# Optimization experiments

Hardware: AMD Instinct MI355X
Metric: run time of the kernel (lower is better)

## Reference

```python
import jax, jax.numpy as jnp
import numpy as np

N = 50000      # nodes
E = 800000     # edges
DIN = 128      # input_dim
H = 128        # hidden_dim
DOUT = 64      # output_dim
G = 256        # graphs in batch
HOPS = 2       # num_hops
EPS = 1e-5     # BatchNorm eps


def setup_inputs() -> dict:
    key = jax.random.key(0)
    ks = jax.random.split(key, 16)
    w = lambda k, shape: jax.random.normal(k, shape, jnp.float32) * 0.05
    return dict(
        x=jax.random.normal(ks[0], (N, DIN), jnp.float32),
        edge_index=jax.random.randint(ks[1], (2, E), 0, N),
        batch=jnp.sort(jax.random.randint(ks[2], (N,), 0, G)),
        # preprocess FFNN (weights stored [in, out]; math == torch x @ W.T + b)
        pre_w1=w(ks[3], (DIN, H)), pre_b1=jnp.zeros((H,), jnp.float32),
        pre_w2=w(ks[4], (H, H)),   pre_b2=jnp.zeros((H,), jnp.float32),
        # per-hop GCNConv weight/bias
        conv_w=w(ks[5], (HOPS, H, H)), conv_b=jnp.zeros((HOPS, H), jnp.float32),
        # per-hop FFNN
        ffnn_w1=w(ks[6], (HOPS, H, H)), ffnn_b1=jnp.zeros((HOPS, H), jnp.float32),
        ffnn_w2=w(ks[7], (HOPS, H, H)), ffnn_b2=jnp.zeros((HOPS, H), jnp.float32),
        # per-hop BatchNorm affine params
        bn_gamma=jnp.ones((HOPS, H), jnp.float32), bn_beta=jnp.zeros((HOPS, H), jnp.float32),
        # postprocess FFNN
        post_w1=w(ks[8], (H, H)),    post_b1=jnp.zeros((H,), jnp.float32),
        post_w2=w(ks[9], (H, DOUT)), post_b2=jnp.zeros((DOUT,), jnp.float32),
    )


def _ffnn(x, w1, b1, w2, b2):
    # Linear -> GELU(exact, erf-based like nn.GELU) -> Linear
    return jax.nn.gelu(x @ w1 + b1, approximate=False) @ w2 + b2


def reference(x, edge_index, batch,
              pre_w1, pre_b1, pre_w2, pre_b2,
              conv_w, conv_b, ffnn_w1, ffnn_b1, ffnn_w2, ffnn_b2,
              bn_gamma, bn_beta,
              post_w1, post_b1, post_w2, post_b2):
    n = x.shape[0]
    loops = jnp.arange(n)
    # GCNConv default: add self-loops, symmetric D^-1/2 A D^-1/2 normalization
    src = jnp.concatenate([edge_index[0], loops])
    dst = jnp.concatenate([edge_index[1], loops])
    deg = jax.ops.segment_sum(jnp.ones(src.shape[0], x.dtype), dst, num_segments=n)
    dis = jnp.where(deg > 0, jax.lax.rsqrt(deg), 0.0)
    norm = dis[src] * dis[dst]  # [E+N]

    x = _ffnn(x, pre_w1, pre_b1, pre_w2, pre_b2)  # preprocess
    for i in range(HOPS):
        # GCNConv: (x W) gathered at src, scaled, scatter-added at dst, + bias
        xw = x @ conv_w[i]
        agg = jax.ops.segment_sum(xw[src] * norm[:, None], dst, num_segments=n) + conv_b[i]
        x = agg + x  # residual
        # BatchNorm1d (training-mode batch statistics, biased variance)
        mean = x.mean(axis=0)
        var = x.var(axis=0)
        x = (x - mean) * jax.lax.rsqrt(var + EPS) * bn_gamma[i] + bn_beta[i]
        # dropout treated as identity (deterministic reference)
        x = _ffnn(x, ffnn_w1[i], ffnn_b1[i], ffnn_w2[i], ffnn_b2[i]) + x
    # global_mean_pool over graph ids
    sums = jax.ops.segment_sum(x, batch, num_segments=G)
    cnt = jax.ops.segment_sum(jnp.ones(n, x.dtype), batch, num_segments=G)
    pooled = sums / jnp.maximum(cnt, 1.0)[:, None]
    return _ffnn(pooled, post_w1, post_b1, post_w2, post_b2)
```

## Files before the change

### kernel.cpp

```cpp
#include <hip/hip_runtime.h>
#include <hip/hip_bf16.h>
#include <math.h>

#define NN 50000
#define EE 800000
#define GG 256

typedef short bf16x8 __attribute__((ext_vector_type(8)));
typedef float f32x4 __attribute__((ext_vector_type(4)));
typedef unsigned int u32x4 __attribute__((ext_vector_type(4)));

__device__ __forceinline__ unsigned short f2bf(float x) {
    __hip_bfloat16 h = __float2bfloat16(x);
    union { __hip_bfloat16 h; unsigned short u; } c; c.h = h; return c.u;
}
__device__ __forceinline__ float bf2f(unsigned short u) {
    union { unsigned int v; float f; } t; t.v = ((unsigned int)u) << 16; return t.f;
}
__device__ __forceinline__ float gelu_f(float v) {
    return 0.5f * v * (1.0f + erff(v * 0.70710678118654752f));
}
__device__ __forceinline__ int swz(int row, int bytecol) {
    return row * 256 + (bytecol ^ ((row & 7) << 4));
}

__global__ void k_deg(const int* __restrict__ dst, int* __restrict__ degi, int E) {
    int i = blockIdx.x * blockDim.x + threadIdx.x;
    if (i < E) atomicAdd(&degi[dst[i]], 1);
}
__global__ void k_scan1(const int* __restrict__ degi, int* __restrict__ incl,
                        int* __restrict__ bsum, int N) {
    __shared__ int sm[1024];
    int t = threadIdx.x, i = blockIdx.x * 1024 + t;
    int v = (i < N) ? degi[i] : 0;
    sm[t] = v;
    __syncthreads();
    for (int off = 1; off < 1024; off <<= 1) {
        int add = (t >= off) ? sm[t - off] : 0;
        __syncthreads();
        sm[t] += add;
        __syncthreads();
    }
    if (i < N) incl[i] = sm[t];
    if (t == 1023) bsum[blockIdx.x] = sm[t];
}
__global__ void k_scan3(const int* __restrict__ incl, const int* __restrict__ degi,
                        const int* __restrict__ bsum, float* __restrict__ dis,
                        int* __restrict__ rowstart, int N, int E, int nsb) {
    __shared__ int sboff;
    int t = threadIdx.x;
    if (t < 64) {
        int nb = blockIdx.x >> 2;
        int v = (t < nb && t < nsb) ? bsum[t] : 0;
        #pragma unroll
        for (int o = 1; o < 64; o <<= 1) v += __shfl_xor(v, o, 64);
        if (t == 0) sboff = v;
    }
    __syncthreads();
    int i = blockIdx.x * 256 + t;
    if (i < N) {
        rowstart[i] = incl[i] - degi[i] + sboff;
        dis[i] = rsqrtf((float)(degi[i] + 1));
    }
    if (i == 0) rowstart[N] = E;
}
__global__ void k_fill(const int* __restrict__ src, const int* __restrict__ dst,
                       const int* __restrict__ rowstart,
                       int* __restrict__ fillc, int* __restrict__ col, int E) {
    int i = blockIdx.x * blockDim.x + threadIdx.x;
    if (i < E) {
        int s = src[i], d = dst[i];
        int pos = rowstart[d] + atomicAdd(&fillc[d], 1);
        col[pos] = s;
    }
}
__global__ void k_prepw8(const float* __restrict__ w0, const float* __restrict__ w1,
                         const float* __restrict__ w2, const float* __restrict__ w3,
                         const float* __restrict__ w4, const float* __restrict__ w5,
                         const float* __restrict__ w6, const float* __restrict__ w7,
                         unsigned short* __restrict__ Wt) {
    int b = blockIdx.x >> 6;
    const float* W = b == 0 ? w0 : b == 1 ? w1 : b == 2 ? w2 : b == 3 ? w3
                   : b == 4 ? w4 : b == 5 ? w5 : b == 6 ? w6 : w7;
    int tid = (blockIdx.x & 63) * 256 + threadIdx.x;
    int n = tid >> 7, k = tid & 127;
    *(unsigned short*)((char*)(Wt + (size_t)b * 16384) + swz(n, k * 2)) = f2bf(W[k * 128 + n]);
}

__global__ __launch_bounds__(256) void k_mm(
    const float* __restrict__ A32, const unsigned short* __restrict__ A16,
    const unsigned short* __restrict__ W1, const float* __restrict__ b1,
    const unsigned short* __restrict__ W2, const float* __restrict__ b2,
    const unsigned short* __restrict__ W3, const float* __restrict__ disv,
    const float* __restrict__ st_sum, const float* __restrict__ st_sq,
    const float* __restrict__ st_g, const float* __restrict__ st_b,
    float invN, int bn, int hasres,
    float* __restrict__ outx32, unsigned short* __restrict__ out3,
    const int* __restrict__ batch, float* __restrict__ pooled, int M)
{
    __shared__ unsigned short As[64 * 128];
    __shared__ unsigned short Ws[128 * 128];
    __shared__ float lsc[128], lsh[128];
    __shared__ float sdis[64];
    __shared__ int gid[64];
    const int tid = threadIdx.x;
    const int bm = blockIdx.x * 64;
    if (st_sum && tid < 128) {
        float m = st_sum[tid] * invN;
        float var = st_sq[tid] * invN - m * m;
        float s = st_g[tid] * rsqrtf(var + 1e-5f);
        lsc[tid] = s;
        lsh[tid] = st_b[tid] - m * s;
    }
    __syncthreads();
    {
        const uint4* srcp = (const uint4*)W1;
        uint4* dstp = (uint4*)Ws;
        for (int i = tid; i < 2048; i += 256) dstp[i] = srcp[i];
    }
    #pragma unroll
    for (int pass = 0; pass < 4; ++pass) {
        int row = pass * 16 + (tid >> 4);
        int c8 = tid & 15;
        int gr = bm + row; if (gr > M - 1) gr = M - 1;
        float vv[8];
        if (A32) {
            const float* pp = A32 + (size_t)gr * 128 + c8 * 8;
            float4 v0 = *(const float4*)pp;
            float4 v1 = *(const float4*)(pp + 4);
            vv[0] = v0.x; vv[1] = v0.y; vv[2] = v0.z; vv[3] = v0.w;
            vv[4] = v1.x; vv[5] = v1.y; vv[6] = v1.z; vv[7] = v1.w;
        } else {
            u32x4 raw = __builtin_nontemporal_load((const u32x4*)(A16 + (size_t)gr * 128 + c8 * 8));
            #pragma unroll
            for (int d = 0; d < 4; ++d) {
                vv[2 * d]     = bf2f((unsigned short)(raw[d] & 0xffff));
                vv[2 * d + 1] = bf2f((unsigned short)(raw[d] >> 16));
            }
        }
        if (bn) {
            int ch = c8 * 8;
            #pragma unroll
            for (int j = 0; j < 8; ++j) vv[j] = vv[j] * lsc[ch + j] + lsh[ch + j];
        }
        unsigned short tmp[8];
        #pragma unroll
        for (int j = 0; j < 8; ++j) tmp[j] = f2bf(vv[j]);
        *(uint4*)((char*)As + swz(row, c8 * 16)) = *(uint4*)tmp;
    }
    __syncthreads();

    const int lane = tid & 63, wid = tid >> 6;
    const int r0 = wid * 16;
    const int lrow = lane & 15;
    const int lkb = (lane >> 4) * 16;
    const int cb = lane & 15;
    const int rb = r0 + (lane >> 4) * 4;

    f32x4 acc[8];
    #pragma unroll
    for (int n = 0; n < 8; ++n) acc[n] = (f32x4){0.f, 0.f, 0.f, 0.f};
    #pragma unroll
    for (int kk = 0; kk < 4; ++kk) {
        int bc = kk * 64 + lkb;
        bf16x8 a = *(const bf16x8*)((const char*)As + swz(r0 + lrow, bc));
        #pragma unroll
        for (int n = 0; n < 8; ++n) {
            bf16x8 b = *(const bf16x8*)((const char*)Ws + swz(n * 16 + lrow, bc));
            acc[n] = __builtin_amdgcn_mfma_f32_16x16x32_bf16(a, b, acc[n], 0, 0, 0);
        }
    }
    unsigned short rres[32];
    if (hasres) {
        #pragma unroll
        for (int n = 0; n < 8; ++n)
            #pragma unroll
            for (int j = 0; j < 4; ++j)
                rres[n * 4 + j] = *(const unsigned short*)((const char*)As + swz(rb + j, (n * 16 + cb) * 2));
    }
    #pragma unroll
    for (int n = 0; n < 8; ++n) {
        int colg = n * 16 + cb;
        float bv = b1[colg];
        #pragma unroll
        for (int j = 0; j < 4; ++j) {
            float v = gelu_f(acc[n][j] + bv);
            *(unsigned short*)((char*)As + swz(rb + j, colg * 2)) = f2bf(v);
        }
    }
    __syncthreads();
    {
        const uint4* srcp = (const uint4*)W2;
        uint4* dstp = (uint4*)Ws;
        for (int i = tid; i < 2048; i += 256) dstp[i] = srcp[i];
    }
    __syncthreads();
    #pragma unroll
    for (int n = 0; n < 8; ++n) acc[n] = (f32x4){0.f, 0.f, 0.f, 0.f};
    #pragma unroll
    for (int kk = 0; kk < 4; ++kk) {
        int bc = kk * 64 + lkb;
        bf16x8 a = *(const bf16x8*)((const char*)As + swz(r0 + lrow, bc));
        #pragma unroll
        for (int n = 0; n < 8; ++n) {
            bf16x8 b = *(const bf16x8*)((const char*)Ws + swz(n * 16 + lrow, bc));
            acc[n] = __builtin_amdgcn_mfma_f32_16x16x32_bf16(a, b, acc[n], 0, 0, 0);
        }
    }
    const int dopool = (pooled != nullptr);
    float* wsf = (float*)Ws;
    #pragma unroll
    for (int n = 0; n < 8; ++n) {
        int colg = n * 16 + cb;
        float bv = b2[colg];
        #pragma unroll
        for (int j = 0; j < 4; ++j) {
            int rowg = bm + rb + j;
            float v = acc[n][j] + bv;
            if (hasres) v += bf2f(rres[n * 4 + j]);
            if (outx32 && rowg < M) outx32[(size_t)rowg * 128 + colg] = v;
            if (W3) *(unsigned short*)((char*)As + swz(rb + j, colg * 2)) = f2bf(v);
            if (dopool) wsf[(rb + j) * 128 + colg] = v;
        }
    }
    if (dopool) {
        if (tid < 64) { int r = bm + tid; gid[tid] = (r < M) ? batch[r] : -1; }
        __syncthreads();
        if (tid < 128) {
            float pacc = 0.f;
            int gcur = gid[0];
            #pragma unroll 4
            for (int r = 0; r < 64; ++r) {
                int gg = gid[r];
                if (gg != gcur) {
                    if (gcur >= 0) atomicAdd(&pooled[(size_t)gcur * 128 + tid], pacc);
                    pacc = 0.f; gcur = gg;
                }
                if (gg >= 0) pacc += wsf[r * 128 + tid];
            }
            if (gcur >= 0) atomicAdd(&pooled[(size_t)gcur * 128 + tid], pacc);
        }
        return;
    }
    if (!W3) return;
    __syncthreads();
    {
        const uint4* srcp = (const uint4*)W3;
        uint4* dstp = (uint4*)Ws;
        for (int i = tid; i < 2048; i += 256) dstp[i] = srcp[i];
        if (tid < 64) { int r = bm + tid; sdis[tid] = disv[(r < M) ? r : (M - 1)]; }
    }
    __syncthreads();
    #pragma unroll
    for (int n = 0; n < 8; ++n) acc[n] = (f32x4){0.f, 0.f, 0.f, 0.f};
    #pragma unroll
    for (int kk = 0; kk < 4; ++kk) {
        int bc = kk * 64 + lkb;
        bf16x8 a = *(const bf16x8*)((const char*)As + swz(r0 + lrow, bc));
        #pragma unroll
        for (int n = 0; n < 8; ++n) {
            bf16x8 b = *(const bf16x8*)((const char*)Ws + swz(n * 16 + lrow, bc));
            acc[n] = __builtin_amdgcn_mfma_f32_16x16x32_bf16(a, b, acc[n], 0, 0, 0);
        }
    }
    #pragma unroll
    for (int n = 0; n < 8; ++n) {
        int colg = n * 16 + cb;
        #pragma unroll
        for (int j = 0; j < 4; ++j) {
            int rowg = bm + rb + j;
            if (rowg < M) out3[(size_t)rowg * 128 + colg] = f2bf(acc[n][j] * sdis[rb + j]);
        }
    }
}

__global__ __launch_bounds__(256) void k_agg(
    const unsigned short* __restrict__ xws, const int* __restrict__ rowstart,
    const int* __restrict__ col,
    const float* __restrict__ dis, const float* __restrict__ convb,
    const float* __restrict__ x0, unsigned short* __restrict__ zbf,
    float* __restrict__ bnsum, float* __restrict__ bnsq, int N)
{
    __shared__ float redS[4][128];
    __shared__ float redQ[4][128];
    const int tid = threadIdx.x;
    const int lane = tid & 63;
    const int wid = tid >> 6;
    const int g = lane >> 4;
    const int cl = lane & 15;
    const int ch = cl * 8;
    const int wave = blockIdx.x * 4 + wid;
    const int nwaves = gridDim.x * 4;

    float cb[8];
    #pragma unroll
    for (int j = 0; j < 8; ++j) cb[j] = convb[ch + j];
    float s[8], q[8];
    #pragma unroll
    for (int j = 0; j < 8; ++j) { s[j] = 0.f; q[j] = 0.f; }

    for (int v = wave; v < N; v += nwaves) {
        const int e0 = rowstart[v], e1 = rowstart[v + 1];
        float a[8];
        #pragma unroll
        for (int j = 0; j < 8; ++j) a[j] = 0.f;
        int e = e0 + g;
        for (; e + 12 < e1; e += 16) {
            const int u0 = col[e];
            const int u1 = col[e + 4];
            const int u2 = col[e + 8];
            const int u3 = col[e + 12];
            u32x4 p0 = *(const u32x4*)(xws + (size_t)u0 * 128 + ch);
            u32x4 p1 = *(const u32x4*)(xws + (size_t)u1 * 128 + ch);
            u32x4 p2 = *(const u32x4*)(xws + (size_t)u2 * 128 + ch);
            u32x4 p3 = *(const u32x4*)(xws + (size_t)u3 * 128 + ch);
            #pragma unroll
            for (int d = 0; d < 4; ++d) {
                a[2 * d]     += bf2f((unsigned short)(p0[d] & 0xffff)) + bf2f((unsigned short)(p1[d] & 0xffff))
                              + bf2f((unsigned short)(p2[d] & 0xffff)) + bf2f((unsigned short)(p3[d] & 0xffff));
                a[2 * d + 1] += bf2f((unsigned short)(p0[d] >> 16)) + bf2f((unsigned short)(p1[d] >> 16))
                              + bf2f((unsigned short)(p2[d] >> 16)) + bf2f((unsigned short)(p3[d] >> 16));
            }
        }
        for (; e + 4 < e1; e += 8) {
            const int u0 = col[e];
            const int u1 = col[e + 4];
            u32x4 p0 = *(const u32x4*)(xws + (size_t)u0 * 128 + ch);
            u32x4 p1 = *(const u32x4*)(xws + (size_t)u1 * 128 + ch);
            #pragma unroll
            for (int d = 0; d < 4; ++d) {
                a[2 * d]     += bf2f((unsigned short)(p0[d] & 0xffff)) + bf2f((unsigned short)(p1[d] & 0xffff));
                a[2 * d + 1] += bf2f((unsigned short)(p0[d] >> 16)) + bf2f((unsigned short)(p1[d] >> 16));
            }
        }
        if (e < e1) {
            const int u = col[e];
            u32x4 p = *(const u32x4*)(xws + (size_t)u * 128 + ch);
            #pragma unroll
            for (int d = 0; d < 4; ++d) {
                a[2 * d]     += bf2f((unsigned short)(p[d] & 0xffff));
                a[2 * d + 1] += bf2f((unsigned short)(p[d] >> 16));
            }
        }
        #pragma unroll
        for (int j = 0; j < 8; ++j) {
            a[j] += __shfl_xor(a[j], 16, 64);
            a[j] += __shfl_xor(a[j], 32, 64);
        }
        if (g == 0) {
            const float dv = dis[v];
            u32x4 p = *(const u32x4*)(xws + (size_t)v * 128 + ch);
            f32x4 xa = __builtin_nontemporal_load((const f32x4*)(x0 + (size_t)v * 128 + ch));
            f32x4 xb = __builtin_nontemporal_load((const f32x4*)(x0 + (size_t)v * 128 + ch + 4));
            const float xr[8] = { xa[0], xa[1], xa[2], xa[3], xb[0], xb[1], xb[2], xb[3] };
            float zz[8];
            #pragma unroll
            for (int d = 0; d < 4; ++d) {
                zz[2 * d]     = dv * (a[2 * d]     + bf2f((unsigned short)(p[d] & 0xffff)));
                zz[2 * d + 1] = dv * (a[2 * d + 1] + bf2f((unsigned short)(p[d] >> 16)));
            }
            unsigned short zo[8];
            #pragma unroll
            for (int j = 0; j < 8; ++j) {
                zz[j] += cb[j] + xr[j];
                s[j] += zz[j];
                q[j] += zz[j] * zz[j];
                zo[j] = f2bf(zz[j]);
            }
            __builtin_nontemporal_store(*(const u32x4*)zo, (u32x4*)(zbf + (size_t)v * 128 + ch));
        }
    }
    if (g == 0) {
        #pragma unroll
        for (int j = 0; j < 8; ++j) { redS[wid][ch + j] = s[j]; redQ[wid][ch + j] = q[j]; }
    }
    __syncthreads();
    if (tid < 128) {
        float ts = redS[0][tid] + redS[1][tid] + redS[2][tid] + redS[3][tid];
        float tq = redQ[0][tid] + redQ[1][tid] + redQ[2][tid] + redQ[3][tid];
        atomicAdd(&bnsum[tid], ts);
        atomicAdd(&bnsq[tid], tq);
    }
}
__global__ __launch_bounds__(128) void k_post(
    const float* __restrict__ pooled, const int* __restrict__ batch,
    const float* __restrict__ w1, const float* __restrict__ b1,
    const float* __restrict__ w2, const float* __restrict__ b2,
    float* __restrict__ out, int N, int G)
{
    __shared__ float pr[128], hr[128];
    __shared__ int bounds[2];
    int g = blockIdx.x, t = threadIdx.x;
    if (t < 2) {
        int tgt = g + t, lo = 0, hi = N;
        while (lo < hi) { int mid = (lo + hi) >> 1; if (batch[mid] < tgt) lo = mid + 1; else hi = mid; }
        bounds[t] = lo;
    }
    __syncthreads();
    float c = fmaxf((float)(bounds[1] - bounds[0]), 1.0f);
    pr[t] = pooled[(size_t)g * 128 + t] / c;
    __syncthreads();
    float a = b1[t];
    for (int k = 0; k < 128; ++k) a += pr[k] * w1[k * 128 + t];
    hr[t] = gelu_f(a);
    __syncthreads();
    if (t < 64) {
        float o = b2[t];
        for (int k = 0; k < 128; ++k) o += hr[k] * w2[k * 64 + t];
        out[g * 64 + t] = o;
    }
}

extern "C" void kernel_launch(void* const* d_in, const int* in_sizes, int n_in,
                              void* d_out, int out_size, void* d_ws, size_t ws_size,
                              hipStream_t stream) {
    (void)in_sizes; (void)n_in; (void)out_size; (void)ws_size;
    const float* x_in    = (const float*)d_in[0];
    const int*   ei      = (const int*)d_in[1];
    const int*   batch   = (const int*)d_in[2];
    const float* pre_w1  = (const float*)d_in[3];
    const float* pre_b1  = (const float*)d_in[4];
    const float* pre_w2  = (const float*)d_in[5];
    const float* pre_b2  = (const float*)d_in[6];
    const float* conv_w  = (const float*)d_in[7];
    const float* conv_b  = (const float*)d_in[8];
    const float* ffnn_w1 = (const float*)d_in[9];
    const float* ffnn_b1 = (const float*)d_in[10];
    const float* ffnn_w2 = (const float*)d_in[11];
    const float* ffnn_b2 = (const float*)d_in[12];
    const float* bn_gamma= (const float*)d_in[13];
    const float* bn_beta = (const float*)d_in[14];
    const float* post_w1 = (const float*)d_in[15];
    const float* post_b1 = (const float*)d_in[16];
    const float* post_w2 = (const float*)d_in[17];
    const float* post_b2 = (const float*)d_in[18];
    const int* srcE = ei;
    const int* dstE = ei + EE;

    char* base = (char*)d_ws;
    size_t off = 0;
    auto carve = [&](size_t bytes) {
        char* q = base + off;
        off = (off + bytes + 255) & ~(size_t)255;
        return q;
    };
    float* xf32 = (float*)carve((size_t)NN * 128 * 4);
    unsigned short* zbf = (unsigned short*)carve((size_t)NN * 128 * 2);
    unsigned short* hbf = (unsigned short*)carve((size_t)NN * 128 * 2);
    float* dis   = (float*)carve((size_t)NN * 4);
    int*   degi  = (int*)carve((size_t)NN * 4);
    int*   fillc = (int*)carve((size_t)NN * 4);
    float* pooled= (float*)carve((size_t)GG * 128 * 4);
    float* bnstat= (float*)carve(512 * 4);
    size_t zlen  = (size_t)((char*)(bnstat + 512) - (char*)degi);
    int* incl    = (int*)carve((size_t)NN * 4);
    int* bsum    = (int*)carve(64 * 4);
    int* rowstart= (int*)carve((size_t)(NN + 1) * 4);
    int* colx    = (int*)carve((size_t)EE * 4);
    unsigned short* Wt = (unsigned short*)carve((size_t)8 * 16384 * 2);

    hipMemsetAsync(degi, 0, zlen, stream);

    const int nsb = (NN + 1023) / 1024;
    k_deg<<<(EE + 255) / 256, 256, 0, stream>>>(dstE, degi, EE);
    k_scan1<<<nsb, 1024, 0, stream>>>(degi, incl, bsum, NN);
    k_scan3<<<(NN + 255) / 256, 256, 0, stream>>>(incl, degi, bsum, dis, rowstart, NN, EE, nsb);
    k_fill<<<(EE + 255) / 256, 256, 0, stream>>>(srcE, dstE, rowstart, fillc, colx, EE);
    k_prepw8<<<512, 256, 0, stream>>>(pre_w1, pre_w2, conv_w, conv_w + 16384,
                                      ffnn_w1, ffnn_w1 + 16384, ffnn_w2, ffnn_w2 + 16384, Wt);

    const int gB = (NN + 63) / 64;
    const float invN = 1.0f / NN;
    k_mm<<<gB, 256, 0, stream>>>(x_in, nullptr, Wt + 0 * 16384, pre_b1, Wt + 1 * 16384, pre_b2,
                                 Wt + 2 * 16384, dis, nullptr, nullptr, nullptr, nullptr,
                                 invN, 0, 0, xf32, hbf, nullptr, nullptr, NN);
    k_agg<<<2048, 256, 0, stream>>>(hbf, rowstart, colx, dis, conv_b,
                                    xf32, zbf, bnstat, bnstat + 128, NN);
    k_mm<<<gB, 256, 0, stream>>>(nullptr, zbf, Wt + 4 * 16384, ffnn_b1, Wt + 6 * 16384, ffnn_b2,
                                 Wt + 3 * 16384, dis, bnstat, bnstat + 128, bn_gamma, bn_beta,
                                 invN, 1, 1, xf32, hbf, nullptr, nullptr, NN);
    k_agg<<<2048, 256, 0, stream>>>(hbf, rowstart, colx, dis, conv_b + 128,
                                    xf32, zbf, bnstat + 256, bnstat + 384, NN);
    k_mm<<<gB, 256, 0, stream>>>(nullptr, zbf, Wt + 5 * 16384, ffnn_b1 + 128, Wt + 7 * 16384, ffnn_b2 + 128,
                                 nullptr, nullptr, bnstat + 256, bnstat + 384, bn_gamma + 128, bn_beta + 128,
                                 invN, 1, 1, nullptr, nullptr, batch, pooled, NN);
    k_post<<<GG, 128, 0, stream>>>(pooled, batch, post_w1, post_b1, post_w2, post_b2,
                                   (float*)d_out, NN, GG);
}
```

Before: 381.9 us.

## Store residual stream in bf16, merge fill and weight-prep kernels, hoist agg loads

The fp32 residual activation buffer becomes bf16, which halves the bytes k_mm writes and k_agg reads for the residual. The CSR fill and weight-prep kernels are merged into one launch to save launch overhead. In k_agg the self-term and residual loads are issued before the neighbour loop so their latency overlaps the gather. The pooling path now stages results in shared memory after a barrier rather than inside the epilogue, and the bf16 residual adds rounding error.

```diff
diff --git a/kernel.cpp b/kernel.cpp
--- a/kernel.cpp
+++ b/kernel.cpp
@@ -5,6 +5,7 @@
 #define NN 50000
 #define EE 800000
 #define GG 256
+#define FILLB ((EE + 255) / 256)
 
 typedef short bf16x8 __attribute__((ext_vector_type(8)));
 typedef float f32x4 __attribute__((ext_vector_type(4)));
@@ -64,27 +65,30 @@
     }
     if (i == 0) rowstart[N] = E;
 }
-__global__ void k_fill(const int* __restrict__ src, const int* __restrict__ dst,
-                       const int* __restrict__ rowstart,
-                       int* __restrict__ fillc, int* __restrict__ col, int E) {
-    int i = blockIdx.x * blockDim.x + threadIdx.x;
-    if (i < E) {
-        int s = src[i], d = dst[i];
-        int pos = rowstart[d] + atomicAdd(&fillc[d], 1);
-        col[pos] = s;
-    }
-}
-__global__ void k_prepw8(const float* __restrict__ w0, const float* __restrict__ w1,
-                         const float* __restrict__ w2, const float* __restrict__ w3,
-                         const float* __restrict__ w4, const float* __restrict__ w5,
-                         const float* __restrict__ w6, const float* __restrict__ w7,
-                         unsigned short* __restrict__ Wt) {
-    int b = blockIdx.x >> 6;
-    const float* W = b == 0 ? w0 : b == 1 ? w1 : b == 2 ? w2 : b == 3 ? w3
-                   : b == 4 ? w4 : b == 5 ? w5 : b == 6 ? w6 : w7;
-    int tid = (blockIdx.x & 63) * 256 + threadIdx.x;
-    int n = tid >> 7, k = tid & 127;
-    *(unsigned short*)((char*)(Wt + (size_t)b * 16384) + swz(n, k * 2)) = f2bf(W[k * 128 + n]);
+__global__ void k_fillprep(const int* __restrict__ src, const int* __restrict__ dst,
+                           const int* __restrict__ rowstart, int* __restrict__ fillc,
+                           int* __restrict__ col,
+                           const float* __restrict__ w0, const float* __restrict__ w1,
+                           const float* __restrict__ w2, const float* __restrict__ w3,
+                           const float* __restrict__ w4, const float* __restrict__ w5,
+                           const float* __restrict__ w6, const float* __restrict__ w7,
+                           unsigned short* __restrict__ Wt, int E) {
+    int blk = blockIdx.x;
+    if (blk < FILLB) {
+        int i = blk * 256 + threadIdx.x;
+        if (i < E) {
+            int s = src[i], d = dst[i];
+            int pos = rowstart[d] + atomicAdd(&fillc[d], 1);
+            col[pos] = s;
+        }
+    } else {
+        int b = (blk - FILLB) >> 6;
+        const float* W = b == 0 ? w0 : b == 1 ? w1 : b == 2 ? w2 : b == 3 ? w3
+                       : b == 4 ? w4 : b == 5 ? w5 : b == 6 ? w6 : w7;
+        int tid = ((blk - FILLB) & 63) * 256 + threadIdx.x;
+        int n = tid >> 7, k = tid & 127;
+        *(unsigned short*)((char*)(Wt + (size_t)b * 16384) + swz(n, k * 2)) = f2bf(W[k * 128 + n]);
+    }
 }
 
 __global__ __launch_bounds__(256) void k_mm(
@@ -95,7 +99,7 @@
     const float* __restrict__ st_sum, const float* __restrict__ st_sq,
     const float* __restrict__ st_g, const float* __restrict__ st_b,
     float invN, int bn, int hasres,
-    float* __restrict__ outx32, unsigned short* __restrict__ out3,
+    unsigned short* __restrict__ outxbf, unsigned short* __restrict__ out3,
     const int* __restrict__ batch, float* __restrict__ pooled, int M)
 {
     __shared__ unsigned short As[64 * 128];
@@ -208,7 +212,6 @@
         }
     }
     const int dopool = (pooled != nullptr);
-    float* wsf = (float*)Ws;
     #pragma unroll
     for (int n = 0; n < 8; ++n) {
         int colg = n * 16 + cb;
@@ -218,12 +221,19 @@
             int rowg = bm + rb + j;
             float v = acc[n][j] + bv;
             if (hasres) v += bf2f(rres[n * 4 + j]);
-            if (outx32 && rowg < M) outx32[(size_t)rowg * 128 + colg] = v;
+            acc[n][j] = v;
+            if (outxbf && rowg < M) outxbf[(size_t)rowg * 128 + colg] = f2bf(v);
             if (W3) *(unsigned short*)((char*)As + swz(rb + j, colg * 2)) = f2bf(v);
-            if (dopool) wsf[(rb + j) * 128 + colg] = v;
         }
     }
     if (dopool) {
+        __syncthreads();
+        float* wsf = (float*)Ws;
+        #pragma unroll
+        for (int n = 0; n < 8; ++n)
+            #pragma unroll
+            for (int j = 0; j < 4; ++j)
+                wsf[(rb + j) * 128 + n * 16 + cb] = acc[n][j];
         if (tid < 64) { int r = bm + tid; gid[tid] = (r < M) ? batch[r] : -1; }
         __syncthreads();
         if (tid < 128) {
@@ -278,7 +288,7 @@
     const unsigned short* __restrict__ xws, const int* __restrict__ rowstart,
     const int* __restrict__ col,
     const float* __restrict__ dis, const float* __restrict__ convb,
-    const float* __restrict__ x0, unsigned short* __restrict__ zbf,
+    const unsigned short* __restrict__ x0, unsigned short* __restrict__ zbf,
     float* __restrict__ bnsum, float* __restrict__ bnsq, int N)
 {
     __shared__ float redS[4][128];
@@ -301,6 +311,14 @@
 
     for (int v = wave; v < N; v += nwaves) {
         const int e0 = rowstart[v], e1 = rowstart[v + 1];
+        float dv = 0.f;
+        u32x4 pself = (u32x4){0, 0, 0, 0};
+        u32x4 x16 = (u32x4){0, 0, 0, 0};
+        if (g == 0) {
+            dv = dis[v];
+            pself = *(const u32x4*)(xws + (size_t)v * 128 + ch);
+            x16 = __builtin_nontemporal_load((const u32x4*)(x0 + (size_t)v * 128 + ch));
+        }
         float a[8];
         #pragma unroll
         for (int j = 0; j < 8; ++j) a[j] = 0.f;
@@ -348,17 +366,18 @@
             a[j] += __shfl_xor(a[j], 32, 64);
         }
         if (g == 0) {
-            const float dv = dis[v];
-            u32x4 p = *(const u32x4*)(xws + (size_t)v * 128 + ch);
-            f32x4 xa = __builtin_nontemporal_load((const f32x4*)(x0 + (size_t)v * 128 + ch));
-            f32x4 xb = __builtin_nontemporal_load((const f32x4*)(x0 + (size_t)v * 128 + ch + 4));
-            const float xr[8] = { xa[0], xa[1], xa[2], xa[3], xb[0], xb[1], xb[2], xb[3] };
             float zz[8];
             #pragma unroll
             for (int d = 0; d < 4; ++d) {
-                zz[2 * d]     = dv * (a[2 * d]     + bf2f((unsigned short)(p[d] & 0xffff)));
-                zz[2 * d + 1] = dv * (a[2 * d + 1] + bf2f((unsigned short)(p[d] >> 16)));
-            }
+                zz[2 * d]     = dv * (a[2 * d]     + bf2f((unsigned short)(pself[d] & 0xffff)));
+                zz[2 * d + 1] = dv * (a[2 * d + 1] + bf2f((unsigned short)(pself[d] >> 16)));
+            }
+            const float xr[8] = {
+                bf2f((unsigned short)(x16[0] & 0xffff)), bf2f((unsigned short)(x16[0] >> 16)),
+                bf2f((unsigned short)(x16[1] & 0xffff)), bf2f((unsigned short)(x16[1] >> 16)),
+                bf2f((unsigned short)(x16[2] & 0xffff)), bf2f((unsigned short)(x16[2] >> 16)),
+                bf2f((unsigned short)(x16[3] & 0xffff)), bf2f((unsigned short)(x16[3] >> 16))
+            };
             unsigned short zo[8];
             #pragma unroll
             for (int j = 0; j < 8; ++j) {
@@ -444,7 +463,7 @@
         off = (off + bytes + 255) & ~(size_t)255;
         return q;
     };
-    float* xf32 = (float*)carve((size_t)NN * 128 * 4);
+    unsigned short* xbf = (unsigned short*)carve((size_t)NN * 128 * 2);
     unsigned short* zbf = (unsigned short*)carve((size_t)NN * 128 * 2);
     unsigned short* hbf = (unsigned short*)carve((size_t)NN * 128 * 2);
     float* dis   = (float*)carve((size_t)NN * 4);
@@ -465,22 +484,23 @@
     k_deg<<<(EE + 255) / 256, 256, 0, stream>>>(dstE, degi, EE);
     k_scan1<<<nsb, 1024, 0, stream>>>(degi, incl, bsum, NN);
     k_scan3<<<(NN + 255) / 256, 256, 0, stream>>>(incl, degi, bsum, dis, rowstart, NN, EE, nsb);
-    k_fill<<<(EE + 255) / 256, 256, 0, stream>>>(srcE, dstE, rowstart, fillc, colx, EE);
-    k_prepw8<<<512, 256, 0, stream>>>(pre_w1, pre_w2, conv_w, conv_w + 16384,
-                                      ffnn_w1, ffnn_w1 + 16384, ffnn_w2, ffnn_w2 + 16384, Wt);
+    k_fillprep<<<FILLB + 512, 256, 0, stream>>>(srcE, dstE, rowstart, fillc, colx,
+                                                pre_w1, pre_w2, conv_w, conv_w + 16384,
+                                                ffnn_w1, ffnn_w1 + 16384, ffnn_w2, ffnn_w2 + 16384,
+                                                Wt, EE);
 
     const int gB = (NN + 63) / 64;
     const float invN = 1.0f / NN;
     k_mm<<<gB, 256, 0, stream>>>(x_in, nullptr, Wt + 0 * 16384, pre_b1, Wt + 1 * 16384, pre_b2,
                                  Wt + 2 * 16384, dis, nullptr, nullptr, nullptr, nullptr,
-                                 invN, 0, 0, xf32, hbf, nullptr, nullptr, NN);
+                                 invN, 0, 0, xbf, hbf, nullptr, nullptr, NN);
     k_agg<<<2048, 256, 0, stream>>>(hbf, rowstart, colx, dis, conv_b,
-                                    xf32, zbf, bnstat, bnstat + 128, NN);
+                                    xbf, zbf, bnstat, bnstat + 128, NN);
     k_mm<<<gB, 256, 0, stream>>>(nullptr, zbf, Wt + 4 * 16384, ffnn_b1, Wt + 6 * 16384, ffnn_b2,
                                  Wt + 3 * 16384, dis, bnstat, bnstat + 128, bn_gamma, bn_beta,
-                                 invN, 1, 1, xf32, hbf, nullptr, nullptr, NN);
+                                 invN, 1, 1, xbf, hbf, nullptr, nullptr, NN);
     k_agg<<<2048, 256, 0, stream>>>(hbf, rowstart, colx, dis, conv_b + 128,
-                                    xf32, zbf, bnstat + 256, bnstat + 384, NN);
+                                    xbf, zbf, bnstat + 256, bnstat + 384, NN);
     k_mm<<<gB, 256, 0, stream>>>(nullptr, zbf, Wt + 5 * 16384, ffnn_b1 + 128, Wt + 7 * 16384, ffnn_b2 + 128,
                                  nullptr, nullptr, bnstat + 256, bnstat + 384, bn_gamma + 128, bn_beta + 128,
                                  invN, 1, 1, nullptr, nullptr, batch, pooled, NN);
```

Measured after the change: 370.5 us. -3.0%, faster.
